# Performance work log

Hardware: AMD Instinct MI355X
Metric: run time of the kernel (lower is better)

Reference implementation:

```python
import jax, jax.numpy as jnp
import numpy as np

B, S, D, H = 4, 2048, 1024, 16
HD = D // H

def setup_inputs() -> dict:
    key = jax.random.key(0)
    ks = jax.random.split(key, 10)
    s = 1.0 / np.sqrt(D)
    inp = {
        'x': jax.random.normal(ks[0], (B, S, D), dtype=jnp.float32),
        'attention_mask': jnp.ones((B, S), dtype=jnp.int32),
        'Wq': jax.random.uniform(ks[1], (D, D), jnp.float32, -s, s),
        'bq': jax.random.uniform(ks[2], (D,), jnp.float32, -s, s),
        'Wk': jax.random.uniform(ks[3], (D, D), jnp.float32, -s, s),
        'bk': jax.random.uniform(ks[4], (D,), jnp.float32, -s, s),
        'Wv': jax.random.uniform(ks[5], (D, D), jnp.float32, -s, s),
        'bv': jax.random.uniform(ks[6], (D,), jnp.float32, -s, s),
        'Wo': jax.random.uniform(ks[7], (D, D), jnp.float32, -s, s),
        'bo': jax.random.uniform(ks[8], (D,), jnp.float32, -s, s),
    }
    return inp

def reference(x, Wq, bq, Wk, bk, Wv, bv, Wo, bo, attention_mask):
    scale = HD ** -0.5
    # torch Linear: y = x @ W^T + b
    def proj(W, b):
        return (x @ W.T + b).reshape(B, S, H, HD).transpose(0, 2, 1, 3)  # [B,H,S,hd]
    q = proj(Wq, bq)
    k = proj(Wk, bk)
    v = proj(Wv, bv)
    scores = jnp.einsum('bhqd,bhkd->bhqk', q, k) * scale  # [B,H,S,S]
    causal = jnp.triu(jnp.ones((S, S), dtype=bool), k=1)
    scores = jnp.where(causal, -jnp.inf, scores)
    pad = (attention_mask == 0)[:, None, None, :]  # [B,1,1,S]
    scores = jnp.where(pad, jnp.float32(-1e9), scores)
    probs = jax.nn.softmax(scores, axis=-1)
    out = jnp.einsum('bhqk,bhkd->bhqd', probs, v)  # [B,H,S,hd]
    out = out.transpose(0, 2, 1, 3).reshape(B, S, D)
    return out @ Wo.T + bo
```

## Files before the change

### kernel.cpp

```cpp
#include <hip/hip_runtime.h>
#include <hip/hip_bf16.h>

typedef unsigned short u16;
typedef float f32x4 __attribute__((ext_vector_type(4)));
typedef __bf16 bf16x8 __attribute__((ext_vector_type(8)));

#define BB 4
#define SS 2048
#define DD 1024
#define HH 16
#define HDD 64
#define MM (BB*SS)

__device__ __forceinline__ u16 f2bf(float f){
    union { float f; unsigned int i; } v; v.f = f;
    unsigned int i = v.i;
    return (u16)((i + 0x7FFFu + ((i >> 16) & 1u)) >> 16);
}
__device__ __forceinline__ ushort2 pk2(float a, float b){
    union { __hip_bfloat162 h; ushort2 u; } v;
    float2 t; t.x = a; t.y = b;
    v.h = __float22bfloat162_rn(t);
    return v.u;
}
__device__ __forceinline__ ushort4 pk4(float a, float b, float c, float d){
    ushort2 lo = pk2(a, b), hi = pk2(c, d);
    ushort4 r; r.x = lo.x; r.y = lo.y; r.z = hi.x; r.w = hi.y;
    return r;
}
__device__ __forceinline__ void gl2lds16(const void* g, void* l){
    __builtin_amdgcn_global_load_lds(
        (const __attribute__((address_space(1))) void*)g,
        (__attribute__((address_space(3))) void*)l, 16, 0, 0);
}

__global__ __launch_bounds__(256) void cvt_k(const float* __restrict__ src,
                                             u16* __restrict__ dst)
{
    const size_t i = ((size_t)blockIdx.x * 256 + threadIdx.x) * 8;
    const float4 a = *(const float4*)&src[i];
    const float4 b = *(const float4*)&src[i + 4];
    ushort4 lo = pk4(a.x, a.y, a.z, a.w);
    ushort4 hi = pk4(b.x, b.y, b.z, b.w);
    uint4 o;
    o.x = (unsigned)lo.x | ((unsigned)lo.y << 16);
    o.y = (unsigned)lo.z | ((unsigned)lo.w << 16);
    o.z = (unsigned)hi.x | ((unsigned)hi.y << 16);
    o.w = (unsigned)hi.z | ((unsigned)hi.w << 16);
    *(uint4*)&dst[i] = o;
}

__device__ __forceinline__ void gemm_core(const u16* __restrict__ A,
                                          const float* __restrict__ W,
                                          f32x4 (&acc)[4][4],
                                          u16* At, u16* Bt,
                                          int m0, int n0, int tid)
{
    const int lane = tid & 63, w = tid >> 6;
    const int quad = lane >> 4, l15 = lane & 15;
    const int wm = w >> 1, wn = w & 1;
    const int arow = lane >> 2;
    const int acol = (lane & 3) * 8;

    for (int k0 = 0; k0 < DD; k0 += 32) {
        __syncthreads();
        #pragma unroll
        for (int c = 0; c < 2; ++c) {
            const int ch = w * 2 + c;
            gl2lds16(&A[(size_t)(m0 + ch * 16 + arow) * DD + k0 + acol], &At[ch * 512]);
        }
        #pragma unroll
        for (int it = 0; it < 2; ++it) {
            const int c = tid + it * 256;
            const int row = c >> 2, cc = (c & 3) * 8;
            const size_t woff = (size_t)(n0 + row) * DD + k0 + cc;
            const float4 u0 = *(const float4*)&W[woff];
            const float4 u1 = *(const float4*)&W[woff + 4];
            ushort4 lo = pk4(u0.x, u0.y, u0.z, u0.w);
            ushort4 hi = pk4(u1.x, u1.y, u1.z, u1.w);
            uint4 o;
            o.x = (unsigned)lo.x | ((unsigned)lo.y << 16);
            o.y = (unsigned)lo.z | ((unsigned)lo.w << 16);
            o.z = (unsigned)hi.x | ((unsigned)hi.y << 16);
            o.w = (unsigned)hi.z | ((unsigned)hi.w << 16);
            *(uint4*)&Bt[row * 32 + cc] = o;
        }
        __syncthreads();
        bf16x8 af[4], bfr[4];
        #pragma unroll
        for (int i = 0; i < 4; ++i)
            af[i] = *(const bf16x8*)&At[(wm * 64 + i * 16 + l15) * 32 + quad * 8];
        #pragma unroll
        for (int j = 0; j < 4; ++j)
            bfr[j] = *(const bf16x8*)&Bt[(wn * 64 + j * 16 + l15) * 32 + quad * 8];
        #pragma unroll
        for (int i = 0; i < 4; ++i)
            #pragma unroll
            for (int j = 0; j < 4; ++j)
                acc[i][j] = __builtin_amdgcn_mfma_f32_16x16x32_bf16(af[i], bfr[j], acc[i][j], 0, 0, 0);
    }
}

__global__ __launch_bounds__(256, 4) void gemm_qkv_k(
    const u16* __restrict__ x,
    const float* __restrict__ Wq, const float* __restrict__ bq,
    const float* __restrict__ Wk, const float* __restrict__ bk,
    const float* __restrict__ Wv, const float* __restrict__ bv,
    u16* __restrict__ Q, u16* __restrict__ K, u16* __restrict__ V)
{
    __shared__ alignas(16) u16 At[128 * 32];
    __shared__ alignas(16) u16 Bt[128 * 32];
    const int tid = threadIdx.x, lane = tid & 63, w = tid >> 6;
    const int quad = lane >> 4, l15 = lane & 15;
    const int wm = w >> 1, wn = w & 1;
    const int z = blockIdx.z;
    const float* Wm = z == 0 ? Wq : (z == 1 ? Wk : Wv);
    const float* bias = z == 0 ? bq : (z == 1 ? bk : bv);
    u16* Out = z == 0 ? Q : (z == 1 ? K : V);
    const int m0 = blockIdx.x * 128, n0 = blockIdx.y * 128;

    f32x4 acc[4][4];
    #pragma unroll
    for (int i = 0; i < 4; ++i)
        #pragma unroll
        for (int j = 0; j < 4; ++j) acc[i][j] = (f32x4)(0.0f);

    gemm_core(x, Wm, acc, At, Bt, m0, n0, tid);

    float bs[4];
    #pragma unroll
    for (int j = 0; j < 4; ++j) bs[j] = bias[n0 + wn * 64 + j * 16 + l15];

    const int b = m0 / SS;
    const int h = (n0 + wn * 64) / HDD;
    const size_t base = ((size_t)(b * HH + h)) * SS * HDD;
    #pragma unroll
    for (int i = 0; i < 4; ++i) {
        #pragma unroll
        for (int r = 0; r < 4; ++r) {
            const int s = (m0 % SS) + wm * 64 + i * 16 + quad * 4 + r;
            #pragma unroll
            for (int j = 0; j < 4; ++j) {
                const int hd = j * 16 + l15;
                Out[base + (size_t)s * HDD + hd] = f2bf(acc[i][j][r] + bs[j]);
            }
        }
    }
}

__global__ __launch_bounds__(256, 4) void gemm_out_k(
    const u16* __restrict__ A, const float* __restrict__ Wo,
    const float* __restrict__ bo, float* __restrict__ Out)
{
    __shared__ alignas(16) u16 At[128 * 32];
    __shared__ alignas(16) u16 Bt[128 * 32];
    const int tid = threadIdx.x, lane = tid & 63, w = tid >> 6;
    const int quad = lane >> 4, l15 = lane & 15;
    const int wm = w >> 1, wn = w & 1;
    const int m0 = blockIdx.x * 128, n0 = blockIdx.y * 128;

    f32x4 acc[4][4];
    #pragma unroll
    for (int i = 0; i < 4; ++i)
        #pragma unroll
        for (int j = 0; j < 4; ++j) acc[i][j] = (f32x4)(0.0f);

    gemm_core(A, Wo, acc, At, Bt, m0, n0, tid);

    float bs[4];
    #pragma unroll
    for (int j = 0; j < 4; ++j) bs[j] = bo[n0 + wn * 64 + j * 16 + l15];

    #pragma unroll
    for (int i = 0; i < 4; ++i) {
        #pragma unroll
        for (int r = 0; r < 4; ++r) {
            const int m = m0 + wm * 64 + i * 16 + quad * 4 + r;
            #pragma unroll
            for (int j = 0; j < 4; ++j) {
                const int n = n0 + wn * 64 + j * 16 + l15;
                Out[(size_t)m * DD + n] = acc[i][j][r] + bs[j];
            }
        }
    }
}

#define QT 256
#define KT 64
#define LDP 72
#define LDPV 66

#define LOG2E 1.4426950408889634f

__global__ __launch_bounds__(512, 2) void attn_k(
    const u16* __restrict__ Q, const u16* __restrict__ K,
    const u16* __restrict__ V, const int* __restrict__ mask,
    u16* __restrict__ AO)
{
    __shared__ alignas(16) u16 QPs[QT * LDP];
    __shared__ alignas(16) u16 Ks[KT * LDP];
    __shared__ alignas(16) u16 Vs[HDD * LDPV];
    __shared__ float padf[KT];

    const int tid = threadIdx.x, lane = tid & 63, w = tid >> 6;
    const int quad = lane >> 4, l15 = lane & 15;
    const int bh = blockIdx.x;
    const int y = blockIdx.y;
    const int qt = (y < 4) ? (7 - y) : (y - 4);
    const int b = bh >> 4, h = bh & 15;
    const int q0 = qt * QT;
    const size_t hoff = (size_t)bh * SS * HDD;
    const u16* Qh = Q + hoff;
    const u16* Kh = K + hoff;
    const u16* Vh = V + hoff;

    for (int c = tid; c < QT * 8; c += 512) {
        const int row = c >> 3, cc = c & 7;
        *(uint4*)&QPs[row * LDP + cc * 8] = *(const uint4*)&Qh[(size_t)(q0 + row) * HDD + cc * 8];
    }
    __syncthreads();
    bf16x8 bQ[2][2];
    #pragma unroll
    for (int j = 0; j < 2; ++j)
        #pragma unroll
        for (int ks = 0; ks < 2; ++ks)
            bQ[j][ks] = *(const bf16x8*)&QPs[(w * 32 + j * 16 + l15) * LDP + ks * 32 + quad * 8];

    float m_run[2] = { -1e30f, -1e30f };
    float l_run[2] = { 0.f, 0.f };
    f32x4 o[4][2];
    #pragma unroll
    for (int i = 0; i < 4; ++i)
        #pragma unroll
        for (int j = 0; j < 2; ++j) o[i][j] = (f32x4)(0.0f);

    const int nkt = (q0 + QT) / KT;
    const float scale2 = 0.125f * LOG2E;

    for (int kt = 0; kt < nkt; ++kt) {
        const int kt0 = kt * KT;
        __syncthreads();

        if (tid < 256) {
            #pragma unroll
            for (int it = 0; it < 2; ++it) {
                const int c = tid + it * 256;
                const int row = c >> 3, cc = c & 7;
                *(uint4*)&Ks[row * LDP + cc * 8] = *(const uint4*)&Kh[(size_t)(kt0 + row) * HDD + cc * 8];
            }
        } else if (tid < 384) {
            const int t = tid - 256;
            const int kq = t >> 3;
            const int c0 = (t & 7) * 8;
            uint4 r0 = *(const uint4*)&Vh[(size_t)(kt0 + kq * 4 + 0) * HDD + c0];
            uint4 r1 = *(const uint4*)&Vh[(size_t)(kt0 + kq * 4 + 1) * HDD + c0];
            uint4 r2 = *(const uint4*)&Vh[(size_t)(kt0 + kq * 4 + 2) * HDD + c0];
            uint4 r3 = *(const uint4*)&Vh[(size_t)(kt0 + kq * 4 + 3) * HDD + c0];
            const u16* e0 = (const u16*)&r0;
            const u16* e1 = (const u16*)&r1;
            const u16* e2 = (const u16*)&r2;
            const u16* e3 = (const u16*)&r3;
            #pragma unroll
            for (int e = 0; e < 8; ++e) {
                ushort4 pkv; pkv.x = e0[e]; pkv.y = e1[e]; pkv.z = e2[e]; pkv.w = e3[e];
                *(ushort4*)&Vs[(c0 + e) * LDPV + kq * 4] = pkv;
            }
        } else if (tid < 448) {
            const int t = tid - 384;
            padf[t] = (mask[b * SS + kt0 + t] == 0) ? 1.0f : 0.0f;
        }
        __syncthreads();

        f32x4 sc[4][2];
        #pragma unroll
        for (int i = 0; i < 4; ++i)
            #pragma unroll
            for (int j = 0; j < 2; ++j) sc[i][j] = (f32x4)(0.0f);
        #pragma unroll
        for (int ks = 0; ks < 2; ++ks) {
            bf16x8 aK[4];
            #pragma unroll
            for (int i = 0; i < 4; ++i)
                aK[i] = *(const bf16x8*)&Ks[(i * 16 + l15) * LDP + ks * 32 + quad * 8];
            #pragma unroll
            for (int i = 0; i < 4; ++i)
                #pragma unroll
                for (int j = 0; j < 2; ++j)
                    sc[i][j] = __builtin_amdgcn_mfma_f32_16x16x32_bf16(aK[i], bQ[j][ks], sc[i][j], 0, 0, 0);
        }

        float pf[4][4];
        #pragma unroll
        for (int i = 0; i < 4; ++i)
            #pragma unroll
            for (int r = 0; r < 4; ++r)
                pf[i][r] = padf[i * 16 + quad * 4 + r];

        #pragma unroll
        for (int j = 0; j < 2; ++j) {
            const int qrow = q0 + w * 32 + j * 16 + l15;
            const bool needC = (kt0 + KT - 1) > (q0 + w * 32 + j * 16);
            float mx = -1e9f;
            if (needC) {
                #pragma unroll
                for (int i = 0; i < 4; ++i)
                    #pragma unroll
                    for (int r = 0; r < 4; ++r) {
                        const int kpg = kt0 + i * 16 + quad * 4 + r;
                        float s = sc[i][j][r] * scale2;
                        s = ((kpg > qrow) || (pf[i][r] != 0.f)) ? -1e9f : s;
                        sc[i][j][r] = s; mx = fmaxf(mx, s);
                    }
            } else {
                #pragma unroll
                for (int i = 0; i < 4; ++i)
                    #pragma unroll
                    for (int r = 0; r < 4; ++r) {
                        float s = sc[i][j][r] * scale2;
                        s = (pf[i][r] != 0.f) ? -1e9f : s;
                        sc[i][j][r] = s; mx = fmaxf(mx, s);
                    }
            }
            mx = fmaxf(mx, __shfl_xor(mx, 16, 64));
            mx = fmaxf(mx, __shfl_xor(mx, 32, 64));
            const float nm = fmaxf(m_run[j], mx);
            const float alpha = __builtin_exp2f(m_run[j] - nm);
            m_run[j] = nm;
            float rs = 0.f;
            #pragma unroll
            for (int i = 0; i < 4; ++i) {
                float p0 = __builtin_exp2f(sc[i][j][0] - nm);
                float p1 = __builtin_exp2f(sc[i][j][1] - nm);
                float p2 = __builtin_exp2f(sc[i][j][2] - nm);
                float p3 = __builtin_exp2f(sc[i][j][3] - nm);
                rs += (p0 + p1) + (p2 + p3);
                *(ushort4*)&QPs[(w * 32 + j * 16 + l15) * LDP + i * 16 + quad * 4] = pk4(p0, p1, p2, p3);
            }
            l_run[j] = l_run[j] * alpha + rs;
            #pragma unroll
            for (int i = 0; i < 4; ++i)
                #pragma unroll
                for (int r = 0; r < 4; ++r) o[i][j][r] *= alpha;
        }
        asm volatile("s_waitcnt lgkmcnt(0)" ::: "memory");

        #pragma unroll
        for (int ks = 0; ks < 2; ++ks) {
            bf16x8 aV[4], bP[2];
            #pragma unroll
            for (int i = 0; i < 4; ++i)
                aV[i] = *(const bf16x8*)&Vs[(i * 16 + l15) * LDPV + ks * 32 + quad * 8];
            #pragma unroll
            for (int j = 0; j < 2; ++j)
                bP[j] = *(const bf16x8*)&QPs[(w * 32 + j * 16 + l15) * LDP + ks * 32 + quad * 8];
            #pragma unroll
            for (int i = 0; i < 4; ++i)
                #pragma unroll
                for (int j = 0; j < 2; ++j)
                    o[i][j] = __builtin_amdgcn_mfma_f32_16x16x32_bf16(aV[i], bP[j], o[i][j], 0, 0, 0);
        }
    }

    #pragma unroll
    for (int j = 0; j < 2; ++j) {
        float l = l_run[j];
        l += __shfl_xor(l, 16, 64);
        l += __shfl_xor(l, 32, 64);
        const float inv = (l > 0.f) ? (1.f / l) : 0.f;
        const int s = q0 + w * 32 + j * 16 + l15;
        const size_t rb = ((size_t)(b * SS + s)) * DD + h * HDD;
        #pragma unroll
        for (int i = 0; i < 4; ++i)
            *(ushort4*)&AO[rb + i * 16 + quad * 4] =
                pk4(o[i][j][0] * inv, o[i][j][1] * inv, o[i][j][2] * inv, o[i][j][3] * inv);
    }
}

extern "C" void kernel_launch(void* const* d_in, const int* in_sizes, int n_in,
                              void* d_out, int out_size, void* d_ws, size_t ws_size,
                              hipStream_t stream)
{
    const float* x  = (const float*)d_in[0];
    const int* mask = (const int*)d_in[1];
    const float* Wq = (const float*)d_in[2];
    const float* bq = (const float*)d_in[3];
    const float* Wk = (const float*)d_in[4];
    const float* bk = (const float*)d_in[5];
    const float* Wv = (const float*)d_in[6];
    const float* bv = (const float*)d_in[7];
    const float* Wo = (const float*)d_in[8];
    const float* bo = (const float*)d_in[9];
    float* out = (float*)d_out;

    u16* ws = (u16*)d_ws;
    const size_t NE = (size_t)MM * DD;
    if (ws_size < 4 * NE * sizeof(u16)) return;

    u16* Qb = ws;
    u16* Kb = ws + NE;
    u16* Vb = ws + 2 * NE;
    u16* Ab = ws + 3 * NE;

    dim3 blk(256);
    cvt_k<<<dim3(NE / 2048), blk, 0, stream>>>(x, Ab);
    gemm_qkv_k<<<dim3(MM / 128, DD / 128, 3), blk, 0, stream>>>(
        Ab, Wq, bq, Wk, bk, Wv, bv, Qb, Kb, Vb);
    attn_k<<<dim3(BB * HH, SS / QT), dim3(512), 0, stream>>>(Qb, Kb, Vb, mask, Ab);
    gemm_out_k<<<dim3(MM / 128, DD / 128), blk, 0, stream>>>(Ab, Wo, bo, out);
}
```

Baseline: 351.9 us.

## Pre-convert weights to bf16 and double-buffer K/V tiles in attention

Adds a kernel that converts all four weight matrices to bf16 in workspace once per call, so both GEMMs load B tiles with direct global-to-LDS copies instead of converting fp32 weights in every block. The attention kernel double-buffers K/V/mask tiles through registers, issuing the next tile's global loads before computing the current one and dropping one barrier per iteration. It also folds the padding mask into an additive bias via fma, skips the softmax rescale when the running max grows by at most 8 (lazy rescaling), adds MFMA priority hints, and raises the occupancy hint. The changes cost more LDS and registers plus an extra conversion launch, and the weight path depends on workspace size.

```diff
diff --git a/kernel.cpp b/kernel.cpp
--- a/kernel.cpp
+++ b/kernel.cpp
@@ -34,10 +34,9 @@
         (__attribute__((address_space(3))) void*)l, 16, 0, 0);
 }
 
-__global__ __launch_bounds__(256) void cvt_k(const float* __restrict__ src,
-                                             u16* __restrict__ dst)
-{
-    const size_t i = ((size_t)blockIdx.x * 256 + threadIdx.x) * 8;
+__device__ __forceinline__ void cvt8(const float* __restrict__ src,
+                                     u16* __restrict__ dst, size_t i)
+{
     const float4 a = *(const float4*)&src[i];
     const float4 b = *(const float4*)&src[i + 4];
     ushort4 lo = pk4(a.x, a.y, a.z, a.w);
@@ -50,11 +49,32 @@
     *(uint4*)&dst[i] = o;
 }
 
-__device__ __forceinline__ void gemm_core(const u16* __restrict__ A,
-                                          const float* __restrict__ W,
-                                          f32x4 (&acc)[4][4],
-                                          u16* At, u16* Bt,
-                                          int m0, int n0, int tid)
+__global__ __launch_bounds__(256) void cvt_k(const float* __restrict__ src,
+                                             u16* __restrict__ dst)
+{
+    const size_t i = ((size_t)blockIdx.x * 256 + threadIdx.x) * 8;
+    cvt8(src, dst, i);
+}
+
+__global__ __launch_bounds__(256) void cvtw_k(
+    const float* __restrict__ W0, const float* __restrict__ W1,
+    const float* __restrict__ W2, const float* __restrict__ W3,
+    u16* __restrict__ dst)
+{
+    const float* src = blockIdx.y == 0 ? W0 : (blockIdx.y == 1 ? W1 :
+                        (blockIdx.y == 2 ? W2 : W3));
+    u16* d = dst + (size_t)blockIdx.y * (size_t)DD * DD;
+    const size_t i = ((size_t)blockIdx.x * 256 + threadIdx.x) * 8;
+    cvt8(src, d, i);
+}
+
+template<bool WB>
+__device__ __forceinline__ void gemm_core_t(const u16* __restrict__ A,
+                                            const float* __restrict__ Wf,
+                                            const u16* __restrict__ Wb,
+                                            f32x4 (&acc)[4][4],
+                                            u16* At, u16* Bt,
+                                            int m0, int n0, int tid)
 {
     const int lane = tid & 63, w = tid >> 6;
     const int quad = lane >> 4, l15 = lane & 15;
@@ -69,21 +89,29 @@
             const int ch = w * 2 + c;
             gl2lds16(&A[(size_t)(m0 + ch * 16 + arow) * DD + k0 + acol], &At[ch * 512]);
         }
-        #pragma unroll
-        for (int it = 0; it < 2; ++it) {
-            const int c = tid + it * 256;
-            const int row = c >> 2, cc = (c & 3) * 8;
-            const size_t woff = (size_t)(n0 + row) * DD + k0 + cc;
-            const float4 u0 = *(const float4*)&W[woff];
-            const float4 u1 = *(const float4*)&W[woff + 4];
-            ushort4 lo = pk4(u0.x, u0.y, u0.z, u0.w);
-            ushort4 hi = pk4(u1.x, u1.y, u1.z, u1.w);
-            uint4 o;
-            o.x = (unsigned)lo.x | ((unsigned)lo.y << 16);
-            o.y = (unsigned)lo.z | ((unsigned)lo.w << 16);
-            o.z = (unsigned)hi.x | ((unsigned)hi.y << 16);
-            o.w = (unsigned)hi.z | ((unsigned)hi.w << 16);
-            *(uint4*)&Bt[row * 32 + cc] = o;
+        if (WB) {
+            #pragma unroll
+            for (int c = 0; c < 2; ++c) {
+                const int ch = w * 2 + c;
+                gl2lds16(&Wb[(size_t)(n0 + ch * 16 + arow) * DD + k0 + acol], &Bt[ch * 512]);
+            }
+        } else {
+            #pragma unroll
+            for (int it = 0; it < 2; ++it) {
+                const int c = tid + it * 256;
+                const int row = c >> 2, cc = (c & 3) * 8;
+                const size_t woff = (size_t)(n0 + row) * DD + k0 + cc;
+                const float4 u0 = *(const float4*)&Wf[woff];
+                const float4 u1 = *(const float4*)&Wf[woff + 4];
+                ushort4 lo = pk4(u0.x, u0.y, u0.z, u0.w);
+                ushort4 hi = pk4(u1.x, u1.y, u1.z, u1.w);
+                uint4 o;
+                o.x = (unsigned)lo.x | ((unsigned)lo.y << 16);
+                o.y = (unsigned)lo.z | ((unsigned)lo.w << 16);
+                o.z = (unsigned)hi.x | ((unsigned)hi.y << 16);
+                o.w = (unsigned)hi.z | ((unsigned)hi.w << 16);
+                *(uint4*)&Bt[row * 32 + cc] = o;
+            }
         }
         __syncthreads();
         bf16x8 af[4], bfr[4];
@@ -101,11 +129,14 @@
     }
 }
 
+template<bool WB>
 __global__ __launch_bounds__(256, 4) void gemm_qkv_k(
     const u16* __restrict__ x,
     const float* __restrict__ Wq, const float* __restrict__ bq,
     const float* __restrict__ Wk, const float* __restrict__ bk,
     const float* __restrict__ Wv, const float* __restrict__ bv,
+    const u16* __restrict__ Wqb, const u16* __restrict__ Wkb,
+    const u16* __restrict__ Wvb,
     u16* __restrict__ Q, u16* __restrict__ K, u16* __restrict__ V)
 {
     __shared__ alignas(16) u16 At[128 * 32];
@@ -115,6 +146,7 @@
     const int wm = w >> 1, wn = w & 1;
     const int z = blockIdx.z;
     const float* Wm = z == 0 ? Wq : (z == 1 ? Wk : Wv);
+    const u16* Wmb = z == 0 ? Wqb : (z == 1 ? Wkb : Wvb);
     const float* bias = z == 0 ? bq : (z == 1 ? bk : bv);
     u16* Out = z == 0 ? Q : (z == 1 ? K : V);
     const int m0 = blockIdx.x * 128, n0 = blockIdx.y * 128;
@@ -125,7 +157,7 @@
         #pragma unroll
         for (int j = 0; j < 4; ++j) acc[i][j] = (f32x4)(0.0f);
 
-    gemm_core(x, Wm, acc, At, Bt, m0, n0, tid);
+    gemm_core_t<WB>(x, Wm, Wmb, acc, At, Bt, m0, n0, tid);
 
     float bs[4];
     #pragma unroll
@@ -148,9 +180,11 @@
     }
 }
 
+template<bool WB>
 __global__ __launch_bounds__(256, 4) void gemm_out_k(
     const u16* __restrict__ A, const float* __restrict__ Wo,
-    const float* __restrict__ bo, float* __restrict__ Out)
+    const float* __restrict__ bo, const u16* __restrict__ Wob,
+    float* __restrict__ Out)
 {
     __shared__ alignas(16) u16 At[128 * 32];
     __shared__ alignas(16) u16 Bt[128 * 32];
@@ -165,7 +199,7 @@
         #pragma unroll
         for (int j = 0; j < 4; ++j) acc[i][j] = (f32x4)(0.0f);
 
-    gemm_core(A, Wo, acc, At, Bt, m0, n0, tid);
+    gemm_core_t<WB>(A, Wo, Wob, acc, At, Bt, m0, n0, tid);
 
     float bs[4];
     #pragma unroll
@@ -192,15 +226,15 @@
 
 #define LOG2E 1.4426950408889634f
 
-__global__ __launch_bounds__(512, 2) void attn_k(
+__global__ __launch_bounds__(512, 4) void attn_k(
     const u16* __restrict__ Q, const u16* __restrict__ K,
     const u16* __restrict__ V, const int* __restrict__ mask,
     u16* __restrict__ AO)
 {
     __shared__ alignas(16) u16 QPs[QT * LDP];
-    __shared__ alignas(16) u16 Ks[KT * LDP];
-    __shared__ alignas(16) u16 Vs[HDD * LDPV];
-    __shared__ float padf[KT];
+    __shared__ alignas(16) u16 Ks[2][KT * LDP];
+    __shared__ alignas(16) u16 Vs[2][HDD * LDPV];
+    __shared__ alignas(16) float padf[2][KT];
 
     const int tid = threadIdx.x, lane = tid & 63, w = tid >> 6;
     const int quad = lane >> 4, l15 = lane & 15;
@@ -213,12 +247,61 @@
     const u16* Qh = Q + hoff;
     const u16* Kh = K + hoff;
     const u16* Vh = V + hoff;
+    const int nkt = (q0 + QT) / KT;
+    const float scale2 = 0.125f * LOG2E;
+
+    uint4 kr0, kr1, vr0, vr1, vr2, vr3;
+    float pr = 0.f;
+
+    auto LOADT = [&](int kt0) {
+        if (tid < 256) {
+            const int row0 = tid >> 3, cc0 = (tid & 7) * 8;
+            kr0 = *(const uint4*)&Kh[(size_t)(kt0 + row0) * HDD + cc0];
+            const int row1 = (tid + 256) >> 3, cc1 = ((tid + 256) & 7) * 8;
+            kr1 = *(const uint4*)&Kh[(size_t)(kt0 + row1) * HDD + cc1];
+        } else if (tid < 384) {
+            const int t = tid - 256;
+            const int kq = t >> 3, c0 = (t & 7) * 8;
+            vr0 = *(const uint4*)&Vh[(size_t)(kt0 + kq * 4 + 0) * HDD + c0];
+            vr1 = *(const uint4*)&Vh[(size_t)(kt0 + kq * 4 + 1) * HDD + c0];
+            vr2 = *(const uint4*)&Vh[(size_t)(kt0 + kq * 4 + 2) * HDD + c0];
+            vr3 = *(const uint4*)&Vh[(size_t)(kt0 + kq * 4 + 3) * HDD + c0];
+        } else if (tid < 448) {
+            pr = (mask[b * SS + kt0 + (tid - 384)] == 0) ? -1e9f : 0.0f;
+        }
+    };
+    auto WRITET = [&](int bb) {
+        if (tid < 256) {
+            const int row0 = tid >> 3, cc0 = (tid & 7) * 8;
+            *(uint4*)&Ks[bb][row0 * LDP + cc0] = kr0;
+            const int row1 = (tid + 256) >> 3, cc1 = ((tid + 256) & 7) * 8;
+            *(uint4*)&Ks[bb][row1 * LDP + cc1] = kr1;
+        } else if (tid < 384) {
+            const int t = tid - 256;
+            const int kq = t >> 3, c0 = (t & 7) * 8;
+            const u16* e0 = (const u16*)&vr0;
+            const u16* e1 = (const u16*)&vr1;
+            const u16* e2 = (const u16*)&vr2;
+            const u16* e3 = (const u16*)&vr3;
+            #pragma unroll
+            for (int e = 0; e < 8; ++e) {
+                ushort4 pkv; pkv.x = e0[e]; pkv.y = e1[e]; pkv.z = e2[e]; pkv.w = e3[e];
+                *(ushort4*)&Vs[bb][(c0 + e) * LDPV + kq * 4] = pkv;
+            }
+        } else if (tid < 448) {
+            padf[bb][tid - 384] = pr;
+        }
+    };
+
+    LOADT(0);
 
     for (int c = tid; c < QT * 8; c += 512) {
         const int row = c >> 3, cc = c & 7;
         *(uint4*)&QPs[row * LDP + cc * 8] = *(const uint4*)&Qh[(size_t)(q0 + row) * HDD + cc * 8];
     }
+    WRITET(0);
     __syncthreads();
+
     bf16x8 bQ[2][2];
     #pragma unroll
     for (int j = 0; j < 2; ++j)
@@ -234,67 +317,39 @@
         #pragma unroll
         for (int j = 0; j < 2; ++j) o[i][j] = (f32x4)(0.0f);
 
-    const int nkt = (q0 + QT) / KT;
-    const float scale2 = 0.125f * LOG2E;
-
     for (int kt = 0; kt < nkt; ++kt) {
+        const int cur = kt & 1;
         const int kt0 = kt * KT;
-        __syncthreads();
-
-        if (tid < 256) {
-            #pragma unroll
-            for (int it = 0; it < 2; ++it) {
-                const int c = tid + it * 256;
-                const int row = c >> 3, cc = c & 7;
-                *(uint4*)&Ks[row * LDP + cc * 8] = *(const uint4*)&Kh[(size_t)(kt0 + row) * HDD + cc * 8];
-            }
-        } else if (tid < 384) {
-            const int t = tid - 256;
-            const int kq = t >> 3;
-            const int c0 = (t & 7) * 8;
-            uint4 r0 = *(const uint4*)&Vh[(size_t)(kt0 + kq * 4 + 0) * HDD + c0];
-            uint4 r1 = *(const uint4*)&Vh[(size_t)(kt0 + kq * 4 + 1) * HDD + c0];
-            uint4 r2 = *(const uint4*)&Vh[(size_t)(kt0 + kq * 4 + 2) * HDD + c0];
-            uint4 r3 = *(const uint4*)&Vh[(size_t)(kt0 + kq * 4 + 3) * HDD + c0];
-            const u16* e0 = (const u16*)&r0;
-            const u16* e1 = (const u16*)&r1;
-            const u16* e2 = (const u16*)&r2;
-            const u16* e3 = (const u16*)&r3;
-            #pragma unroll
-            for (int e = 0; e < 8; ++e) {
-                ushort4 pkv; pkv.x = e0[e]; pkv.y = e1[e]; pkv.z = e2[e]; pkv.w = e3[e];
-                *(ushort4*)&Vs[(c0 + e) * LDPV + kq * 4] = pkv;
-            }
-        } else if (tid < 448) {
-            const int t = tid - 384;
-            padf[t] = (mask[b * SS + kt0 + t] == 0) ? 1.0f : 0.0f;
-        }
-        __syncthreads();
+        if (kt + 1 < nkt) LOADT(kt0 + KT);
+
+        const u16* KsC = Ks[cur];
+        const u16* VsC = Vs[cur];
+        const float* padfC = padf[cur];
 
         f32x4 sc[4][2];
         #pragma unroll
         for (int i = 0; i < 4; ++i)
             #pragma unroll
             for (int j = 0; j < 2; ++j) sc[i][j] = (f32x4)(0.0f);
+        __builtin_amdgcn_s_setprio(1);
         #pragma unroll
         for (int ks = 0; ks < 2; ++ks) {
             bf16x8 aK[4];
             #pragma unroll
             for (int i = 0; i < 4; ++i)
-                aK[i] = *(const bf16x8*)&Ks[(i * 16 + l15) * LDP + ks * 32 + quad * 8];
+                aK[i] = *(const bf16x8*)&KsC[(i * 16 + l15) * LDP + ks * 32 + quad * 8];
             #pragma unroll
             for (int i = 0; i < 4; ++i)
                 #pragma unroll
                 for (int j = 0; j < 2; ++j)
                     sc[i][j] = __builtin_amdgcn_mfma_f32_16x16x32_bf16(aK[i], bQ[j][ks], sc[i][j], 0, 0, 0);
         }
-
-        float pf[4][4];
+        __builtin_amdgcn_s_setprio(0);
+
+        f32x4 pb[4];
         #pragma unroll
         for (int i = 0; i < 4; ++i)
-            #pragma unroll
-            for (int r = 0; r < 4; ++r)
-                pf[i][r] = padf[i * 16 + quad * 4 + r];
+            pb[i] = *(const f32x4*)&padfC[i * 16 + quad * 4];
 
         #pragma unroll
         for (int j = 0; j < 2; ++j) {
@@ -307,8 +362,8 @@
                     #pragma unroll
                     for (int r = 0; r < 4; ++r) {
                         const int kpg = kt0 + i * 16 + quad * 4 + r;
-                        float s = sc[i][j][r] * scale2;
-                        s = ((kpg > qrow) || (pf[i][r] != 0.f)) ? -1e9f : s;
+                        float s = fmaf(sc[i][j][r], scale2, pb[i][r]);
+                        s = (kpg > qrow) ? -1e9f : s;
                         sc[i][j][r] = s; mx = fmaxf(mx, s);
                     }
             } else {
@@ -316,16 +371,23 @@
                 for (int i = 0; i < 4; ++i)
                     #pragma unroll
                     for (int r = 0; r < 4; ++r) {
-                        float s = sc[i][j][r] * scale2;
-                        s = (pf[i][r] != 0.f) ? -1e9f : s;
+                        float s = fmaf(sc[i][j][r], scale2, pb[i][r]);
                         sc[i][j][r] = s; mx = fmaxf(mx, s);
                     }
             }
             mx = fmaxf(mx, __shfl_xor(mx, 16, 64));
             mx = fmaxf(mx, __shfl_xor(mx, 32, 64));
-            const float nm = fmaxf(m_run[j], mx);
-            const float alpha = __builtin_exp2f(m_run[j] - nm);
-            m_run[j] = nm;
+            float nm = m_run[j];
+            if (!__all(mx <= nm + 8.f)) {
+                nm = fmaxf(nm, mx);
+                const float alpha = __builtin_exp2f(m_run[j] - nm);
+                m_run[j] = nm;
+                l_run[j] *= alpha;
+                #pragma unroll
+                for (int i = 0; i < 4; ++i)
+                    #pragma unroll
+                    for (int r = 0; r < 4; ++r) o[i][j][r] *= alpha;
+            }
             float rs = 0.f;
             #pragma unroll
             for (int i = 0; i < 4; ++i) {
@@ -336,20 +398,17 @@
                 rs += (p0 + p1) + (p2 + p3);
                 *(ushort4*)&QPs[(w * 32 + j * 16 + l15) * LDP + i * 16 + quad * 4] = pk4(p0, p1, p2, p3);
             }
-            l_run[j] = l_run[j] * alpha + rs;
-            #pragma unroll
-            for (int i = 0; i < 4; ++i)
-                #pragma unroll
-                for (int r = 0; r < 4; ++r) o[i][j][r] *= alpha;
+            l_run[j] += rs;
         }
         asm volatile("s_waitcnt lgkmcnt(0)" ::: "memory");
 
+        __builtin_amdgcn_s_setprio(1);
         #pragma unroll
         for (int ks = 0; ks < 2; ++ks) {
             bf16x8 aV[4], bP[2];
             #pragma unroll
             for (int i = 0; i < 4; ++i)
-                aV[i] = *(const bf16x8*)&Vs[(i * 16 + l15) * LDPV + ks * 32 + quad * 8];
+                aV[i] = *(const bf16x8*)&VsC[(i * 16 + l15) * LDPV + ks * 32 + quad * 8];
             #pragma unroll
             for (int j = 0; j < 2; ++j)
                 bP[j] = *(const bf16x8*)&QPs[(w * 32 + j * 16 + l15) * LDP + ks * 32 + quad * 8];
@@ -359,6 +418,10 @@
                 for (int j = 0; j < 2; ++j)
                     o[i][j] = __builtin_amdgcn_mfma_f32_16x16x32_bf16(aV[i], bP[j], o[i][j], 0, 0, 0);
         }
+        __builtin_amdgcn_s_setprio(0);
+
+        if (kt + 1 < nkt) WRITET(cur ^ 1);
+        __syncthreads();
     }
 
     #pragma unroll
@@ -394,7 +457,9 @@
 
     u16* ws = (u16*)d_ws;
     const size_t NE = (size_t)MM * DD;
+    const size_t WE = (size_t)DD * DD;
     if (ws_size < 4 * NE * sizeof(u16)) return;
+    const bool wb = ws_size >= (4 * NE + 4 * WE) * sizeof(u16);
 
     u16* Qb = ws;
     u16* Kb = ws + NE;
@@ -403,8 +468,21 @@
 
     dim3 blk(256);
     cvt_k<<<dim3(NE / 2048), blk, 0, stream>>>(x, Ab);
-    gemm_qkv_k<<<dim3(MM / 128, DD / 128, 3), blk, 0, stream>>>(
-        Ab, Wq, bq, Wk, bk, Wv, bv, Qb, Kb, Vb);
-    attn_k<<<dim3(BB * HH, SS / QT), dim3(512), 0, stream>>>(Qb, Kb, Vb, mask, Ab);
-    gemm_out_k<<<dim3(MM / 128, DD / 128), blk, 0, stream>>>(Ab, Wo, bo, out);
-}
+    if (wb) {
+        u16* Wbase = ws + 4 * NE;
+        cvtw_k<<<dim3(WE / 2048, 4), blk, 0, stream>>>(Wq, Wk, Wv, Wo, Wbase);
+        gemm_qkv_k<true><<<dim3(MM / 128, DD / 128, 3), blk, 0, stream>>>(
+            Ab, Wq, bq, Wk, bk, Wv, bv,
+            Wbase, Wbase + WE, Wbase + 2 * WE, Qb, Kb, Vb);
+        attn_k<<<dim3(BB * HH, SS / QT), dim3(512), 0, stream>>>(Qb, Kb, Vb, mask, Ab);
+        gemm_out_k<true><<<dim3(MM / 128, DD / 128), blk, 0, stream>>>(
+            Ab, Wo, bo, Wbase + 3 * WE, out);
+    } else {
+        gemm_qkv_k<false><<<dim3(MM / 128, DD / 128, 3), blk, 0, stream>>>(
+            Ab, Wq, bq, Wk, bk, Wv, bv,
+            nullptr, nullptr, nullptr, Qb, Kb, Vb);
+        attn_k<<<dim3(BB * HH, SS / QT), dim3(512), 0, stream>>>(Qb, Kb, Vb, mask, Ab);
+        gemm_out_k<false><<<dim3(MM / 128, DD / 128), blk, 0, stream>>>(
+            Ab, Wo, bo, nullptr, out);
+    }
+}
```

Result: slower. 466.4 us (+32.5%).
